# Kernel tuning notes

Hardware: AMD Instinct MI355X
Metric: run time of the kernel (lower is better)

The kernel has to match this reference:

```python
import jax, jax.numpy as jnp
import numpy as np

CODEBOOK_SIZE = 4096
CODE_DIM = 256
N = 65536
COMMITMENT_COST = 0.25


def setup_inputs() -> dict:
    key = jax.random.key(0)
    k1, k2 = jax.random.split(key)
    z_flat = jax.random.normal(k1, (N, CODE_DIM), dtype=jnp.float32)
    # embedding initialized uniform(-1/codebook_size, 1/codebook_size) as in torch module
    emb_weight = jax.random.uniform(
        k2, (CODEBOOK_SIZE, CODE_DIM), dtype=jnp.float32,
        minval=-1.0 / CODEBOOK_SIZE, maxval=1.0 / CODEBOOK_SIZE)
    return {"z_flat": z_flat, "emb_weight": emb_weight}


def reference(z_flat, emb_weight):
    # squared L2 distances: [N, K] = |z|^2 + |e|^2 - 2 z e^T
    distances = (
        jnp.sum(z_flat ** 2, axis=1, keepdims=True)
        + jnp.sum(emb_weight ** 2, axis=1)
        - 2.0 * jnp.matmul(z_flat, emb_weight.T)
    )
    indices = jnp.argmin(distances, axis=1)  # [N]
    quantized = emb_weight[indices]          # [N, code_dim]

    e_latent_loss = jnp.mean((jax.lax.stop_gradient(quantized) - z_flat) ** 2)
    q_latent_loss = jnp.mean((quantized - jax.lax.stop_gradient(z_flat)) ** 2)
    loss = q_latent_loss + COMMITMENT_COST * e_latent_loss

    # straight-through estimator
    quantized_st = z_flat + jax.lax.stop_gradient(quantized - z_flat)
    return (loss, quantized_st, indices)
```

## Files before the change

### kernel.cpp

```cpp
#include <hip/hip_runtime.h>

#define KCODES 4096
#define DIM    256
#define NROWS  65536
#define MARGIN 4.0e-4f
#define DSLACK 3.0e-5f
#define LCAP   4096
#define CPAD   32
#define LSTRIDE (DIM + 4)

typedef unsigned long long u64;
typedef unsigned int  uint;
typedef unsigned short ushort;
typedef __attribute__((ext_vector_type(8))) short bf16x8;
typedef __attribute__((ext_vector_type(4))) float f32x4;

typedef __attribute__((address_space(3))) uint lds_u32_t;
typedef __attribute__((address_space(1))) uint glb_u32_t;

__device__ __forceinline__ void g2lds16(const void* g, void* l) {
    __builtin_amdgcn_global_load_lds((const glb_u32_t*)g, (lds_u32_t*)l, 16, 0, 0);
}

__device__ __forceinline__ float dppmin_quad(float m) {
    m = fminf(m, __int_as_float(__builtin_amdgcn_update_dpp(0, __float_as_int(m), 0xB1, 0xF, 0xF, true)));
    m = fminf(m, __int_as_float(__builtin_amdgcn_update_dpp(0, __float_as_int(m), 0x4E, 0xF, 0xF, true)));
    return m;
}
__device__ __forceinline__ float dppmin_row16(float m) {
    m = fminf(m, __int_as_float(__builtin_amdgcn_update_dpp(0, __float_as_int(m), 0x124, 0xF, 0xF, true)));
    m = fminf(m, __int_as_float(__builtin_amdgcn_update_dpp(0, __float_as_int(m), 0x128, 0xF, 0xF, true)));
    return m;
}
__device__ __forceinline__ uint dppor_row16(uint v) {
    v |= (uint)__builtin_amdgcn_update_dpp(0, (int)v, 0x124, 0xF, 0xF, true);
    v |= (uint)__builtin_amdgcn_update_dpp(0, (int)v, 0x128, 0xF, 0xF, true);
    return v;
}


__device__ __forceinline__ float np_half_sum128(const float4* __restrict__ p4) {
    #pragma clang fp contract(off)
    float4 v0 = p4[0], v1 = p4[1];
    float r0 = v0.x * v0.x, r1 = v0.y * v0.y, r2 = v0.z * v0.z, r3 = v0.w * v0.w;
    float r4 = v1.x * v1.x, r5 = v1.y * v1.y, r6 = v1.z * v1.z, r7 = v1.w * v1.w;
    #pragma unroll
    for (int i = 1; i < 16; ++i) {
        float4 a = p4[2 * i], b = p4[2 * i + 1];
        r0 += a.x * a.x; r1 += a.y * a.y; r2 += a.z * a.z; r3 += a.w * a.w;
        r4 += b.x * b.x; r5 += b.y * b.y; r6 += b.z * b.z; r7 += b.w * b.w;
    }
    return ((r0 + r1) + (r2 + r3)) + ((r4 + r5) + (r6 + r7));
}

__global__ void k_rownorm(const float* __restrict__ src, float* __restrict__ dst, int nrows) {
    int r = blockIdx.x * blockDim.x + threadIdx.x;
    if (r >= nrows) return;
    const float4* p4 = (const float4*)(src + (size_t)r * DIM);
    float s;
    {
        #pragma clang fp contract(off)
        s = np_half_sum128(p4) + np_half_sum128(p4 + 32);
    }
    dst[r] = s;
}

__device__ __forceinline__ float f32_dist(float Cr, float ebc, double accv) {
    #pragma clang fp contract(off)
    float A = Cr + ebc;
    float B = 2.0f * (float)accv;
    return A - B;
}

__device__ __forceinline__ ushort f2bf(float f) {
    uint u = __float_as_uint(f);
    return (ushort)((u + 0x7fffu + ((u >> 16) & 1u)) >> 16);
}

__device__ __forceinline__ uint4 pack8(float4 a, float4 b) {
    uint4 ov;
    ov.x = (uint)f2bf(a.x) | ((uint)f2bf(a.y) << 16);
    ov.y = (uint)f2bf(a.z) | ((uint)f2bf(a.w) << 16);
    ov.z = (uint)f2bf(b.x) | ((uint)f2bf(b.y) << 16);
    ov.w = (uint)f2bf(b.z) | ((uint)f2bf(b.w) << 16);
    return ov;
}


__global__ void k_prep(const float* __restrict__ src, ushort* __restrict__ dst,
                       float* __restrict__ nrm, int nrows) {
    int r = blockIdx.x * blockDim.x + threadIdx.x;
    if (r >= nrows) return;
    const float4* p4 = (const float4*)(src + (size_t)r * DIM);
    uint4* d4 = (uint4*)(dst + (size_t)r * DIM);
    float h[2];
    #pragma unroll
    for (int half = 0; half < 2; ++half) {
        #pragma clang fp contract(off)
        const float4* p = p4 + half * 32;
        float4 v0 = p[0], v1 = p[1];
        d4[half * 16] = pack8(v0, v1);
        float r0 = v0.x * v0.x, r1 = v0.y * v0.y, r2 = v0.z * v0.z, r3 = v0.w * v0.w;
        float r4 = v1.x * v1.x, r5 = v1.y * v1.y, r6 = v1.z * v1.z, r7 = v1.w * v1.w;
        #pragma unroll
        for (int i = 1; i < 16; ++i) {
            float4 a = p[2 * i], b = p[2 * i + 1];
            d4[half * 16 + i] = pack8(a, b);
            r0 += a.x * a.x; r1 += a.y * a.y; r2 += a.z * a.z; r3 += a.w * a.w;
            r4 += b.x * b.x; r5 += b.y * b.y; r6 += b.z * b.z; r7 += b.w * b.w;
        }
        h[half] = ((r0 + r1) + (r2 + r3)) + ((r4 + r5) + (r6 + r7));
    }
    {
        #pragma clang fp contract(off)
        nrm[r] = h[0] + h[1];
    }
}

__global__ void k_init(int* __restrict__ cnt) {
    cnt[blockIdx.x * 256 + threadIdx.x] = 0;
}

__global__ __launch_bounds__(256, 2)
void k_gemm(const ushort* __restrict__ zh, const ushort* __restrict__ eh,
            const float* __restrict__ Crow, const float* __restrict__ eb2,
            float* __restrict__ tk, uint* __restrict__ tk2,
            int* __restrict__ cnt, int* __restrict__ list,
            u64* __restrict__ fkey) {
    __shared__ __align__(16) ushort Bs[2][64 * 256];

    const int t = threadIdx.x;
    const int lane = t & 63;
    const int w = t >> 6;
    const int l15 = lane & 15, l4 = lane >> 4;
    const int row0w = blockIdx.x * 128 + w * 32;

    const char* ebp = (const char*)eh;

    auto stage = [&](int buf, int ct2) {
        const char* base = ebp + (size_t)ct2 * 64 * 512;
        #pragma unroll
        for (int i = 0; i < 8; ++i) {
            int idx = i * 256 + t;
            int code = idx >> 5;
            int c16  = idx & 31;
            int src  = (code << 9) + ((c16 ^ (code & 7)) << 4);
            g2lds16(base + src, (char*)Bs[buf] + idx * 16);
        }
    };

    bf16x8 a[2][8];
    #pragma unroll
    for (int f = 0; f < 2; ++f)
        #pragma unroll
        for (int ks = 0; ks < 8; ++ks)
            a[f][ks] = *(const bf16x8*)&zh[(size_t)(row0w + f * 16 + l15) * 256 + ks * 32 + l4 * 8];

    float crf[8];
    #pragma unroll
    for (int f = 0; f < 2; ++f)
        #pragma unroll
        for (int rg = 0; rg < 4; ++rg)
            crf[f * 4 + rg] = Crow[row0w + f * 16 + l4 * 4 + rg];

    float mprev[8];
    const f32x4 fzero = (f32x4){0.f, 0.f, 0.f, 0.f};
    f32x4 accA[2][4], accB[2][4];
    float ebvA[4], ebvB[4];

    auto ksloop = [&](const ushort* Bb, f32x4 (&acc)[2][4]) {
        #pragma unroll
        for (int ks = 0; ks < 8; ++ks) {
            bf16x8 bfv[4];
            #pragma unroll
            for (int cg = 0; cg < 4; ++cg) {
                int rB = cg * 16 + l15;
                int off = rB * 256 + ((ks * 32 + l4 * 8) ^ ((l15 & 7) << 3));
                bfv[cg] = *(const bf16x8*)&Bb[off];
            }
            __builtin_amdgcn_s_setprio(1);
            #pragma unroll
            for (int f = 0; f < 2; ++f)
                #pragma unroll
                for (int cg = 0; cg < 4; ++cg)
                    acc[f][cg] = __builtin_amdgcn_mfma_f32_16x16x32_bf16(
                        a[f][ks], bfv[cg], ks == 0 ? fzero : acc[f][cg], 0, 0, 0);
            __builtin_amdgcn_s_setprio(0);
        }
    };

    auto epi = [&](f32x4 (&acc)[2][4], const float (&ebv)[4], int ct2, bool odd) {
        #pragma unroll
        for (int f = 0; f < 2; ++f) {
            #pragma unroll
            for (int rg = 0; rg < 4; ++rg) {
                float m =    fmaf(-2.0f, acc[f][0][rg], ebv[0]);
                m = fminf(m, fmaf(-2.0f, acc[f][1][rg], ebv[1]));
                m = fminf(m, fmaf(-2.0f, acc[f][2][rg], ebv[2]));
                m = fminf(m, fmaf(-2.0f, acc[f][3][rg], ebv[3]));
                m = dppmin_quad(m);
                if (!odd) {
                    mprev[f * 4 + rg] = m;
                } else {
                    m = fminf(m, mprev[f * 4 + rg]);
                    float mt = dppmin_row16(m);
                    int q = (int)((m - mt) * 1e5f);
                    q = q > 255 ? 255 : q;
                    uint pk = (uint)q << (8 * (l15 >> 2));
                    pk = dppor_row16(pk);
                    if (l15 == 0) {
                        int grow = row0w + f * 16 + l4 * 4 + rg;
                        int tt = ct2 >> 1;
                        tk [(size_t)tt * NROWS + grow] = crf[f * 4 + rg] + mt;
                        tk2[(size_t)tt * NROWS + grow] = pk;
                    }
                }
            }
        }
    };

    stage(0, 0);
    #pragma unroll
    for (int cg = 0; cg < 4; ++cg) ebvA[cg] = eb2[cg * 16 + l15];
    __syncthreads();

    for (int tp = 0; tp < 32; ++tp) {
        int t0 = 2 * tp;
        stage(1, t0 + 1);
        if (tp > 0) epi(accB, ebvB, t0 - 1, true);
        ksloop(Bs[0], accA);
        __syncthreads();

        if (tp < 31) stage(0, t0 + 2);
        #pragma unroll
        for (int cg = 0; cg < 4; ++cg) ebvB[cg] = eb2[(t0 + 1) * 64 + cg * 16 + l15];
        epi(accA, ebvA, t0, false);
        if (tp < 31) {
            #pragma unroll
            for (int cg = 0; cg < 4; ++cg) ebvA[cg] = eb2[(t0 + 2) * 64 + cg * 16 + l15];
        }
        ksloop(Bs[1], accB);
        __syncthreads();
    }
    epi(accB, ebvB, 63, true);

    __syncthreads();
    if (t < 128) {
        int row = blockIdx.x * 128 + t;
        float tm[32]; uint pkv[32];
        #pragma unroll
        for (int tt = 0; tt < 32; ++tt) {
            tm[tt]  = tk [(size_t)tt * NROWS + row];
            pkv[tt] = tk2[(size_t)tt * NROWS + row];
        }
        float best = tm[0];
        #pragma unroll
        for (int tt = 1; tt < 32; ++tt) best = fminf(best, tm[tt]);
        fkey[row] = ~0ull;
        float cutoff = best + (MARGIN + DSLACK);
        #pragma unroll
        for (int tt = 0; tt < 32; ++tt) {
            #pragma unroll
            for (int p = 0; p < 4; ++p) {
                float v = tm[tt] + (float)((pkv[tt] >> (8 * p)) & 255u) * 1e-5f;
                bool pred = v <= cutoff;
                u64 mask = __ballot(pred);
                if (mask) {
                    int sub = tt * 4 + p;
                    int nq = __popcll(mask);
                    int rank = __popcll(mask & ((1ull << lane) - 1ull));
                    int base = 0;
                    if (lane == 0) base = atomicAdd(&cnt[sub * CPAD], nq);
                    base = __shfl(base, 0, 64);
                    int pos = base + rank;
                    if (pred && pos < LCAP) list[sub * LCAP + pos] = row;
                }
            }
        }
    }
}

__global__ __launch_bounds__(256, 2)
void k_exact(const float* __restrict__ z, const float* __restrict__ e,
             const float* __restrict__ Crow, const float* __restrict__ eb2,
             const int* __restrict__ list, const int* __restrict__ cnt,
             u64* __restrict__ fkey) {
    __shared__ __align__(16) float ex[32][260];
    __shared__ __align__(16) float zx[32][260];
    __shared__ int rows[32];
    __shared__ u64 keytab[32][17];
    const int sub = blockIdx.x;
    const int tile = sub >> 2, qq = sub & 3;
    const int nct = cnt[sub * CPAD];
    const int t = threadIdx.x;
    const int rp = t & 15, cs = t >> 4;

    {
        int cc = t >> 3, c8 = t & 7;
        int gcode = tile * 128 + (cc >> 2) * 16 + qq * 4 + (cc & 3);
        const float4* src = (const float4*)(e + (size_t)gcode * DIM);
        float4* dr = (float4*)ex[cc];
        #pragma unroll
        for (int j = 0; j < 8; ++j) dr[c8 + 8 * j] = src[c8 + 8 * j];
    }
    const int gc0 = tile * 128 + (cs >> 2) * 16 + qq * 4 + (cs & 3);
    const int gc1 = tile * 128 + ((cs >> 2) + 4) * 16 + qq * 4 + (cs & 3);
    const float ebc0 = eb2[gc0];
    const float ebc1 = eb2[gc1];

    for (int base = blockIdx.y * 32; base < nct; base += gridDim.y * 32) {
        __syncthreads();
        if (t < 32) {
            int i = base + t;
            rows[t] = list[sub * LCAP + (i < nct ? i : nct - 1)];
        }
        __syncthreads();
        {
            int rr = t >> 3, c8 = t & 7;
            const float4* src = (const float4*)(z + (size_t)rows[rr] * DIM);
            float4* dr = (float4*)zx[rr];
            #pragma unroll
            for (int j = 0; j < 8; ++j) dr[c8 + 8 * j] = src[c8 + 8 * j];
        }
        __syncthreads();

        double a00 = 0.0, a01 = 0.0, a10 = 0.0, a11 = 0.0;
        const float4* z0 = (const float4*)zx[rp];
        const float4* z1 = (const float4*)zx[rp + 16];
        const float4* e0 = (const float4*)ex[cs];
        const float4* e1 = (const float4*)ex[cs + 16];
        #pragma unroll 8
        for (int d4 = 0; d4 < 64; ++d4) {
            float4 x0 = z0[d4], x1 = z1[d4], y0 = e0[d4], y1 = e1[d4];
            a00 += (double)x0.x * (double)y0.x; a00 += (double)x0.y * (double)y0.y;
            a00 += (double)x0.z * (double)y0.z; a00 += (double)x0.w * (double)y0.w;
            a01 += (double)x0.x * (double)y1.x; a01 += (double)x0.y * (double)y1.y;
            a01 += (double)x0.z * (double)y1.z; a01 += (double)x0.w * (double)y1.w;
            a10 += (double)x1.x * (double)y0.x; a10 += (double)x1.y * (double)y0.y;
            a10 += (double)x1.z * (double)y0.z; a10 += (double)x1.w * (double)y0.w;
            a11 += (double)x1.x * (double)y1.x; a11 += (double)x1.y * (double)y1.y;
            a11 += (double)x1.z * (double)y1.z; a11 += (double)x1.w * (double)y1.w;
        }
        int r0 = rows[rp], r1 = rows[rp + 16];
        float C0 = Crow[r0], C1 = Crow[r1];
        u64 k00 = ((u64)__float_as_uint(f32_dist(C0, ebc0, a00)) << 32) | (u64)gc0;
        u64 k01 = ((u64)__float_as_uint(f32_dist(C0, ebc1, a01)) << 32) | (u64)gc1;
        u64 k10 = ((u64)__float_as_uint(f32_dist(C1, ebc0, a10)) << 32) | (u64)gc0;
        u64 k11 = ((u64)__float_as_uint(f32_dist(C1, ebc1, a11)) << 32) | (u64)gc1;
        keytab[rp][cs]      = k00 < k01 ? k00 : k01;
        keytab[rp + 16][cs] = k10 < k11 ? k10 : k11;
        __syncthreads();
        if (t < 32) {
            u64 kb = keytab[t][0];
            #pragma unroll
            for (int j = 1; j < 16; ++j) {
                u64 k = keytab[t][j];
                kb = k < kb ? k : kb;
            }
            atomicMin((unsigned long long*)&fkey[rows[t]], kb);
        }
    }
}

__global__ __launch_bounds__(256)
void k_gather(const float* __restrict__ z, const float* __restrict__ e,
              const u64* __restrict__ fkey, float* __restrict__ out,
              double* __restrict__ partial) {
    __shared__ double lred[4];
    const int t = threadIdx.x;
    const int row = blockIdx.x * 32 + (t >> 3);
    const int c8 = t & 7;
    const int idx = (int)(fkey[row] & 0xffffffffull);
    if (c8 == 0) out[1 + (size_t)NROWS * DIM + row] = (float)idx;
    const float4* zr = (const float4*)(z + (size_t)row * DIM);
    const float4* er = (const float4*)(e + (size_t)idx * DIM);
    float4* orow = (float4*)(out + 1 + (size_t)row * DIM);
    double lacc = 0.0;
    #pragma unroll
    for (int j = 0; j < 8; ++j) {
        float4 q = er[c8 + 8 * j];
        float4 zv = zr[c8 + 8 * j];
        orow[c8 + 8 * j] = q;
        double d0 = (double)q.x - (double)zv.x;
        double d1 = (double)q.y - (double)zv.y;
        double d2 = (double)q.z - (double)zv.z;
        double d3 = (double)q.w - (double)zv.w;
        lacc += d0 * d0 + d1 * d1 + d2 * d2 + d3 * d3;
    }
    for (int off = 32; off > 0; off >>= 1) lacc += __shfl_down(lacc, off, 64);
    if ((t & 63) == 0) lred[t >> 6] = lacc;
    __syncthreads();
    if (t == 0) partial[blockIdx.x] = lred[0] + lred[1] + lred[2] + lred[3];
}

__global__ void k_finish(const double* __restrict__ partial, float* __restrict__ out, int n) {
    __shared__ double s[256];
    double a = 0.0;
    for (int i = threadIdx.x; i < n; i += 256) a += partial[i];
    s[threadIdx.x] = a;
    __syncthreads();
    for (int off = 128; off > 0; off >>= 1) {
        if (threadIdx.x < off) s[threadIdx.x] += s[threadIdx.x + off];
        __syncthreads();
    }
    if (threadIdx.x == 0)
        out[0] = (float)(1.25 * s[0] / ((double)NROWS * (double)DIM));
}


__global__ __launch_bounds__(256, 1)
void k_main_slow(const float* __restrict__ z, const float* __restrict__ e,
                 const float* __restrict__ Crow, const float* __restrict__ eb2,
                 float* __restrict__ out, double* __restrict__ partial) {
    __shared__ float  zt[64][LSTRIDE];
    __shared__ float  et[64][LSTRIDE];
    __shared__ float  redd[64][17];
    __shared__ int    redi[64][17];
    __shared__ int    bsel[64];
    __shared__ double lred[4];

    const int t  = threadIdx.x;
    const int tx = t & 15;
    const int ty = t >> 4;
    const int row0 = blockIdx.x * 64;

    {
        const float4* zsrc = (const float4*)(z + (size_t)row0 * DIM);
        for (int i = t; i < 64 * (DIM / 4); i += 256) {
            int r = i >> 6, c4 = i & 63;
            *(float4*)&zt[r][c4 * 4] = zsrc[r * (DIM / 4) + c4];
        }
    }
    float Cr[4];
    #pragma unroll
    for (int ri = 0; ri < 4; ++ri) Cr[ri] = Crow[row0 + ty * 4 + ri];
    float bestd[4]; int besti[4];
    #pragma unroll
    for (int ri = 0; ri < 4; ++ri) { bestd[ri] = __int_as_float(0x7f800000); besti[ri] = 0; }

    for (int kt = 0; kt < KCODES / 64; ++kt) {
        __syncthreads();
        {
            const float4* esrc = (const float4*)(e + (size_t)kt * 64 * DIM);
            for (int i = t; i < 64 * (DIM / 4); i += 256) {
                int r = i >> 6, c4 = i & 63;
                *(float4*)&et[r][c4 * 4] = esrc[r * (DIM / 4) + c4];
            }
        }
        __syncthreads();
        double acc[4][4];
        #pragma unroll
        for (int a = 0; a < 4; ++a)
            #pragma unroll
            for (int b = 0; b < 4; ++b) acc[a][b] = 0.0;
        #pragma unroll 4
        for (int d4 = 0; d4 < DIM / 4; ++d4) {
            float4 za[4], ea[4];
            #pragma unroll
            for (int ri = 0; ri < 4; ++ri) za[ri] = *(const float4*)&zt[ty * 4 + ri][d4 * 4];
            #pragma unroll
            for (int ci = 0; ci < 4; ++ci) ea[ci] = *(const float4*)&et[tx + 16 * ci][d4 * 4];
            #pragma unroll
            for (int ri = 0; ri < 4; ++ri)
                #pragma unroll
                for (int ci = 0; ci < 4; ++ci)
                    acc[ri][ci] += (double)za[ri].x * (double)ea[ci].x
                                 + (double)za[ri].y * (double)ea[ci].y
                                 + (double)za[ri].z * (double)ea[ci].z
                                 + (double)za[ri].w * (double)ea[ci].w;
        }
        #pragma unroll
        for (int ci = 0; ci < 4; ++ci) {
            int c = kt * 64 + tx + 16 * ci;
            float ebc = eb2[c];
            #pragma unroll
            for (int ri = 0; ri < 4; ++ri) {
                float d = f32_dist(Cr[ri], ebc, acc[ri][ci]);
                if (d < bestd[ri]) { bestd[ri] = d; besti[ri] = c; }
            }
        }
    }
    __syncthreads();
    #pragma unroll
    for (int ri = 0; ri < 4; ++ri) {
        redd[ty * 4 + ri][tx] = bestd[ri];
        redi[ty * 4 + ri][tx] = besti[ri];
    }
    __syncthreads();
    if (t < 64) {
        float bd = redd[t][0]; int bi = redi[t][0];
        for (int j = 1; j < 16; ++j) {
            float d = redd[t][j]; int i2 = redi[t][j];
            if (d < bd || (d == bd && i2 < bi)) { bd = d; bi = i2; }
        }
        bsel[t] = bi;
        out[1 + (size_t)NROWS * DIM + row0 + t] = (float)bi;
    }
    __syncthreads();
    double lacc = 0.0;
    {
        int r = t >> 2, qd = (t & 3) * 64;
        int bi = bsel[r];
        const float* qrow = e + (size_t)bi * DIM + qd;
        float* orow = out + 1 + (size_t)(row0 + r) * DIM + qd;
        #pragma unroll 4
        for (int d = 0; d < 64; ++d) {
            float qv = qrow[d], zv = zt[r][qd + d];
            double df = (double)qv - (double)zv;
            lacc += df * df;
            orow[d] = qv;
        }
    }
    for (int off = 32; off > 0; off >>= 1) lacc += __shfl_down(lacc, off, 64);
    if ((t & 63) == 0) lred[t >> 6] = lacc;
    __syncthreads();
    if (t == 0) partial[blockIdx.x] = lred[0] + lred[1] + lred[2] + lred[3];
}


extern "C" void kernel_launch(void* const* d_in, const int* in_sizes, int n_in,
                              void* d_out, int out_size, void* d_ws, size_t ws_size,
                              hipStream_t stream) {
    const float* z = (const float*)d_in[0];
    const float* e = (const float*)d_in[1];
    float* out = (float*)d_out;
    char* w = (char*)d_ws;

    size_t o = 0;
    auto take = [&](size_t b) { size_t r = o; o = (o + b + 255) & ~(size_t)255; return r; };
    size_t o_zh = take((size_t)NROWS * DIM * 2);
    size_t o_eh = take((size_t)KCODES * DIM * 2);
    size_t o_cr = take((size_t)NROWS * 4);
    size_t o_eb = take((size_t)KCODES * 4);
    size_t o_tk = take((size_t)32 * NROWS * 4);
    size_t o_t2 = take((size_t)32 * NROWS * 4);
    size_t o_fk = take((size_t)NROWS * 8);
    size_t o_cn = take((size_t)128 * CPAD * 4);
    size_t o_ls = take((size_t)128 * LCAP * 4);
    size_t o_pt = take((size_t)2048 * 8);
    size_t need = o;

    if (ws_size >= need) {
        ushort* zh = (ushort*)(w + o_zh);
        ushort* eh = (ushort*)(w + o_eh);
        float* Cr  = (float*)(w + o_cr);
        float* eb  = (float*)(w + o_eb);
        float* tk  = (float*)(w + o_tk);
        uint*  tk2 = (uint*)(w + o_t2);
        u64*   fk  = (u64*)(w + o_fk);
        int*   cn  = (int*)(w + o_cn);
        int*   ls  = (int*)(w + o_ls);
        double* pt = (double*)(w + o_pt);

        k_prep<<<NROWS / 256, 256, 0, stream>>>(z, zh, Cr, NROWS);
        k_prep<<<KCODES / 256, 256, 0, stream>>>(e, eh, eb, KCODES);
        k_init<<<(128 * CPAD) / 256, 256, 0, stream>>>(cn);
        k_gemm<<<NROWS / 128, 256, 0, stream>>>(zh, eh, Cr, eb, tk, tk2, cn, ls, fk);
        dim3 ge(128, 16);
        k_exact<<<ge, 256, 0, stream>>>(z, e, Cr, eb, ls, cn, fk);
        k_gather<<<NROWS / 32, 256, 0, stream>>>(z, e, fk, out, pt);
        k_finish<<<1, 256, 0, stream>>>(pt, out, 2048);
    } else {
        float* Cr  = (float*)w;
        float* eb  = Cr + NROWS;
        double* pt = (double*)(eb + KCODES);
        k_rownorm<<<NROWS / 256, 256, 0, stream>>>(z, Cr, NROWS);
        k_rownorm<<<KCODES / 256, 256, 0, stream>>>(e, eb, KCODES);
        k_main_slow<<<NROWS / 64, 256, 0, stream>>>(z, e, Cr, eb, out, pt);
        k_finish<<<1, 256, 0, stream>>>(pt, out, NROWS / 64);
    }
}
```

Before: 331.4 us.

## Double rows per GEMM wave, prefetch B fragments, split candidate-list build into kernel

New measurement: 370.1 us. 11.7% more time.

```diff
diff --git a/kernel.cpp b/kernel.cpp
--- a/kernel.cpp
+++ b/kernel.cpp
@@ -121,19 +121,17 @@
     cnt[blockIdx.x * 256 + threadIdx.x] = 0;
 }
 
-__global__ __launch_bounds__(256, 2)
+__global__ __launch_bounds__(256, 1)
 void k_gemm(const ushort* __restrict__ zh, const ushort* __restrict__ eh,
             const float* __restrict__ Crow, const float* __restrict__ eb2,
-            float* __restrict__ tk, uint* __restrict__ tk2,
-            int* __restrict__ cnt, int* __restrict__ list,
-            u64* __restrict__ fkey) {
+            float* __restrict__ tk, uint* __restrict__ tk2) {
     __shared__ __align__(16) ushort Bs[2][64 * 256];
 
     const int t = threadIdx.x;
     const int lane = t & 63;
     const int w = t >> 6;
     const int l15 = lane & 15, l4 = lane >> 4;
-    const int row0w = blockIdx.x * 128 + w * 32;
+    const int row0w = blockIdx.x * 256 + w * 64;
 
     const char* ebp = (const char*)eh;
 
@@ -149,49 +147,57 @@
         }
     };
 
-    bf16x8 a[2][8];
-    #pragma unroll
-    for (int f = 0; f < 2; ++f)
+    bf16x8 a[4][8];
+    #pragma unroll
+    for (int f = 0; f < 4; ++f)
         #pragma unroll
         for (int ks = 0; ks < 8; ++ks)
             a[f][ks] = *(const bf16x8*)&zh[(size_t)(row0w + f * 16 + l15) * 256 + ks * 32 + l4 * 8];
 
-    float crf[8];
-    #pragma unroll
-    for (int f = 0; f < 2; ++f)
+    float crf[16];
+    #pragma unroll
+    for (int f = 0; f < 4; ++f)
         #pragma unroll
         for (int rg = 0; rg < 4; ++rg)
             crf[f * 4 + rg] = Crow[row0w + f * 16 + l4 * 4 + rg];
 
-    float mprev[8];
+    float mprev[16];
     const f32x4 fzero = (f32x4){0.f, 0.f, 0.f, 0.f};
-    f32x4 accA[2][4], accB[2][4];
+    f32x4 accA[4][4], accB[4][4];
     float ebvA[4], ebvB[4];
 
-    auto ksloop = [&](const ushort* Bb, f32x4 (&acc)[2][4]) {
+    auto readB = [&](const ushort* Bb, int ks, int cg) -> bf16x8 {
+        int rB = cg * 16 + l15;
+        int off = rB * 256 + ((ks * 32 + l4 * 8) ^ ((l15 & 7) << 3));
+        return *(const bf16x8*)&Bb[off];
+    };
+
+    auto ksloop = [&](const ushort* Bb, f32x4 (&acc)[4][4]) {
+        bf16x8 bva[4], bvb[4];
+        #pragma unroll
+        for (int cg = 0; cg < 4; ++cg) bva[cg] = readB(Bb, 0, cg);
         #pragma unroll
         for (int ks = 0; ks < 8; ++ks) {
-            bf16x8 bfv[4];
-            #pragma unroll
-            for (int cg = 0; cg < 4; ++cg) {
-                int rB = cg * 16 + l15;
-                int off = rB * 256 + ((ks * 32 + l4 * 8) ^ ((l15 & 7) << 3));
-                bfv[cg] = *(const bf16x8*)&Bb[off];
+            const bf16x8* cur = (ks & 1) ? bvb : bva;
+            bf16x8*       nxt = (ks & 1) ? bva : bvb;
+            if (ks < 7) {
+                #pragma unroll
+                for (int cg = 0; cg < 4; ++cg) nxt[cg] = readB(Bb, ks + 1, cg);
             }
             __builtin_amdgcn_s_setprio(1);
             #pragma unroll
-            for (int f = 0; f < 2; ++f)
+            for (int f = 0; f < 4; ++f)
                 #pragma unroll
                 for (int cg = 0; cg < 4; ++cg)
                     acc[f][cg] = __builtin_amdgcn_mfma_f32_16x16x32_bf16(
-                        a[f][ks], bfv[cg], ks == 0 ? fzero : acc[f][cg], 0, 0, 0);
+                        a[f][ks], cur[cg], ks == 0 ? fzero : acc[f][cg], 0, 0, 0);
             __builtin_amdgcn_s_setprio(0);
         }
     };
 
-    auto epi = [&](f32x4 (&acc)[2][4], const float (&ebv)[4], int ct2, bool odd) {
-        #pragma unroll
-        for (int f = 0; f < 2; ++f) {
+    auto epi = [&](f32x4 (&acc)[4][4], const float (&ebv)[4], int ct2, bool odd) {
+        #pragma unroll
+        for (int f = 0; f < 4; ++f) {
             #pragma unroll
             for (int rg = 0; rg < 4; ++rg) {
                 float m =    fmaf(-2.0f, acc[f][0][rg], ebv[0]);
@@ -243,38 +249,41 @@
         __syncthreads();
     }
     epi(accB, ebvB, 63, true);
-
-    __syncthreads();
-    if (t < 128) {
-        int row = blockIdx.x * 128 + t;
-        float tm[32]; uint pkv[32];
-        #pragma unroll
-        for (int tt = 0; tt < 32; ++tt) {
-            tm[tt]  = tk [(size_t)tt * NROWS + row];
-            pkv[tt] = tk2[(size_t)tt * NROWS + row];
-        }
-        float best = tm[0];
-        #pragma unroll
-        for (int tt = 1; tt < 32; ++tt) best = fminf(best, tm[tt]);
-        fkey[row] = ~0ull;
-        float cutoff = best + (MARGIN + DSLACK);
-        #pragma unroll
-        for (int tt = 0; tt < 32; ++tt) {
-            #pragma unroll
-            for (int p = 0; p < 4; ++p) {
-                float v = tm[tt] + (float)((pkv[tt] >> (8 * p)) & 255u) * 1e-5f;
-                bool pred = v <= cutoff;
-                u64 mask = __ballot(pred);
-                if (mask) {
-                    int sub = tt * 4 + p;
-                    int nq = __popcll(mask);
-                    int rank = __popcll(mask & ((1ull << lane) - 1ull));
-                    int base = 0;
-                    if (lane == 0) base = atomicAdd(&cnt[sub * CPAD], nq);
-                    base = __shfl(base, 0, 64);
-                    int pos = base + rank;
-                    if (pred && pos < LCAP) list[sub * LCAP + pos] = row;
-                }
+}
+
+__global__ void k_lists(const float* __restrict__ tk, const uint* __restrict__ tk2,
+                        int* __restrict__ cnt, int* __restrict__ list,
+                        u64* __restrict__ fkey) {
+    int row = blockIdx.x * 256 + threadIdx.x;
+    int lane = threadIdx.x & 63;
+    float tm[32]; uint pk[32];
+    #pragma unroll
+    for (int tt = 0; tt < 32; ++tt) {
+        tm[tt] = tk [(size_t)tt * NROWS + row];
+        pk[tt] = tk2[(size_t)tt * NROWS + row];
+    }
+    float best = tm[0];
+    #pragma unroll
+    for (int tt = 1; tt < 32; ++tt) best = fminf(best, tm[tt]);
+    fkey[row] = ~0ull;
+    float cutoff = best + (MARGIN + DSLACK);
+
+    #pragma unroll
+    for (int tt = 0; tt < 32; ++tt) {
+        #pragma unroll
+        for (int p = 0; p < 4; ++p) {
+            float v = tm[tt] + (float)((pk[tt] >> (8 * p)) & 255u) * 1e-5f;
+            bool pred = v <= cutoff;
+            u64 mask = __ballot(pred);
+            if (mask) {
+                int sub = tt * 4 + p;
+                int nq = __popcll(mask);
+                int rank = __popcll(mask & ((1ull << lane) - 1ull));
+                int base = 0;
+                if (lane == 0) base = atomicAdd(&cnt[sub * CPAD], nq);
+                base = __shfl(base, 0, 64);
+                int pos = base + rank;
+                if (pred && pos < LCAP) list[sub * LCAP + pos] = row;
             }
         }
     }
@@ -555,7 +564,8 @@
         k_prep<<<NROWS / 256, 256, 0, stream>>>(z, zh, Cr, NROWS);
         k_prep<<<KCODES / 256, 256, 0, stream>>>(e, eh, eb, KCODES);
         k_init<<<(128 * CPAD) / 256, 256, 0, stream>>>(cn);
-        k_gemm<<<NROWS / 128, 256, 0, stream>>>(zh, eh, Cr, eb, tk, tk2, cn, ls, fk);
+        k_gemm<<<NROWS / 256, 256, 0, stream>>>(zh, eh, Cr, eb, tk, tk2);
+        k_lists<<<NROWS / 256, 256, 0, stream>>>(tk, tk2, cn, ls, fk);
         dim3 ge(128, 16);
         k_exact<<<ge, 256, 0, stream>>>(z, e, Cr, eb, ls, cn, fk);
         k_gather<<<NROWS / 32, 256, 0, stream>>>(z, e, fk, out, pt);
```

## Refine candidate filtering to 2-code groups and split list building into separate kernel

Applied to the files above, without the earlier changes.

Measured after the change: 334.5 us. About the same (+0.9%).

```diff
diff --git a/kernel.cpp b/kernel.cpp
--- a/kernel.cpp
+++ b/kernel.cpp
@@ -4,7 +4,8 @@
 #define DIM    256
 #define NROWS  65536
 #define MARGIN 4.0e-4f
-#define DSLACK 3.0e-5f
+#define DSLACK 4.0e-5f
+#define QDELT  4.0e-5f
 #define LCAP   4096
 #define CPAD   32
 #define LSTRIDE (DIM + 4)
@@ -22,17 +23,20 @@
     __builtin_amdgcn_global_load_lds((const glb_u32_t*)g, (lds_u32_t*)l, 16, 0, 0);
 }
 
-__device__ __forceinline__ float dppmin_quad(float m) {
+__device__ __forceinline__ float dppmin_pair(float m) {
+    m = fminf(m, __int_as_float(__builtin_amdgcn_update_dpp(0, __float_as_int(m), 0xB1, 0xF, 0xF, true)));
+    return m;
+}
+__device__ __forceinline__ float dppmin_row16(float m) {
     m = fminf(m, __int_as_float(__builtin_amdgcn_update_dpp(0, __float_as_int(m), 0xB1, 0xF, 0xF, true)));
     m = fminf(m, __int_as_float(__builtin_amdgcn_update_dpp(0, __float_as_int(m), 0x4E, 0xF, 0xF, true)));
-    return m;
-}
-__device__ __forceinline__ float dppmin_row16(float m) {
     m = fminf(m, __int_as_float(__builtin_amdgcn_update_dpp(0, __float_as_int(m), 0x124, 0xF, 0xF, true)));
     m = fminf(m, __int_as_float(__builtin_amdgcn_update_dpp(0, __float_as_int(m), 0x128, 0xF, 0xF, true)));
     return m;
 }
 __device__ __forceinline__ uint dppor_row16(uint v) {
+    v |= (uint)__builtin_amdgcn_update_dpp(0, (int)v, 0xB1, 0xF, 0xF, true);
+    v |= (uint)__builtin_amdgcn_update_dpp(0, (int)v, 0x4E, 0xF, 0xF, true);
     v |= (uint)__builtin_amdgcn_update_dpp(0, (int)v, 0x124, 0xF, 0xF, true);
     v |= (uint)__builtin_amdgcn_update_dpp(0, (int)v, 0x128, 0xF, 0xF, true);
     return v;
@@ -124,9 +128,7 @@
 __global__ __launch_bounds__(256, 2)
 void k_gemm(const ushort* __restrict__ zh, const ushort* __restrict__ eh,
             const float* __restrict__ Crow, const float* __restrict__ eb2,
-            float* __restrict__ tk, uint* __restrict__ tk2,
-            int* __restrict__ cnt, int* __restrict__ list,
-            u64* __restrict__ fkey) {
+            float* __restrict__ tk, uint* __restrict__ tk2) {
     __shared__ __align__(16) ushort Bs[2][64 * 256];
 
     const int t = threadIdx.x;
@@ -198,15 +200,15 @@
                 m = fminf(m, fmaf(-2.0f, acc[f][1][rg], ebv[1]));
                 m = fminf(m, fmaf(-2.0f, acc[f][2][rg], ebv[2]));
                 m = fminf(m, fmaf(-2.0f, acc[f][3][rg], ebv[3]));
-                m = dppmin_quad(m);
+                m = dppmin_pair(m);
                 if (!odd) {
                     mprev[f * 4 + rg] = m;
                 } else {
                     m = fminf(m, mprev[f * 4 + rg]);
                     float mt = dppmin_row16(m);
-                    int q = (int)((m - mt) * 1e5f);
-                    q = q > 255 ? 255 : q;
-                    uint pk = (uint)q << (8 * (l15 >> 2));
+                    int q = (int)((m - mt) * 2.5e4f);
+                    q = q > 15 ? 15 : q;
+                    uint pk = (uint)q << (4 * (l15 >> 1));
                     pk = dppor_row16(pk);
                     if (l15 == 0) {
                         int grow = row0w + f * 16 + l4 * 4 + rg;
@@ -243,38 +245,41 @@
         __syncthreads();
     }
     epi(accB, ebvB, 63, true);
-
-    __syncthreads();
-    if (t < 128) {
-        int row = blockIdx.x * 128 + t;
-        float tm[32]; uint pkv[32];
-        #pragma unroll
-        for (int tt = 0; tt < 32; ++tt) {
-            tm[tt]  = tk [(size_t)tt * NROWS + row];
-            pkv[tt] = tk2[(size_t)tt * NROWS + row];
-        }
-        float best = tm[0];
-        #pragma unroll
-        for (int tt = 1; tt < 32; ++tt) best = fminf(best, tm[tt]);
-        fkey[row] = ~0ull;
-        float cutoff = best + (MARGIN + DSLACK);
-        #pragma unroll
-        for (int tt = 0; tt < 32; ++tt) {
-            #pragma unroll
-            for (int p = 0; p < 4; ++p) {
-                float v = tm[tt] + (float)((pkv[tt] >> (8 * p)) & 255u) * 1e-5f;
-                bool pred = v <= cutoff;
-                u64 mask = __ballot(pred);
-                if (mask) {
-                    int sub = tt * 4 + p;
-                    int nq = __popcll(mask);
-                    int rank = __popcll(mask & ((1ull << lane) - 1ull));
-                    int base = 0;
-                    if (lane == 0) base = atomicAdd(&cnt[sub * CPAD], nq);
-                    base = __shfl(base, 0, 64);
-                    int pos = base + rank;
-                    if (pred && pos < LCAP) list[sub * LCAP + pos] = row;
-                }
+}
+
+__global__ void k_lists(const float* __restrict__ tk, const uint* __restrict__ tk2,
+                        int* __restrict__ cnt, int* __restrict__ list,
+                        u64* __restrict__ fkey) {
+    int row = blockIdx.x * 256 + threadIdx.x;
+    int lane = threadIdx.x & 63;
+    float tm[32]; uint pk[32];
+    #pragma unroll
+    for (int tt = 0; tt < 32; ++tt) {
+        tm[tt] = tk [(size_t)tt * NROWS + row];
+        pk[tt] = tk2[(size_t)tt * NROWS + row];
+    }
+    float best = tm[0];
+    #pragma unroll
+    for (int tt = 1; tt < 32; ++tt) best = fminf(best, tm[tt]);
+    fkey[row] = ~0ull;
+    float cutoff = best + (MARGIN + DSLACK);
+
+    #pragma unroll
+    for (int tt = 0; tt < 32; ++tt) {
+        #pragma unroll
+        for (int p = 0; p < 8; ++p) {
+            float v = tm[tt] + (float)((pk[tt] >> (4 * p)) & 15u) * QDELT;
+            bool pred = v <= cutoff;
+            u64 mask = __ballot(pred);
+            if (mask) {
+                int sub = tt * 8 + p;
+                int nq = __popcll(mask);
+                int rank = __popcll(mask & ((1ull << lane) - 1ull));
+                int base = 0;
+                if (lane == 0) base = atomicAdd(&cnt[sub * CPAD], nq);
+                base = __shfl(base, 0, 64);
+                int pos = base + rank;
+                if (pred && pos < LCAP) list[sub * LCAP + pos] = row;
             }
         }
     }
@@ -285,28 +290,26 @@
              const float* __restrict__ Crow, const float* __restrict__ eb2,
              const int* __restrict__ list, const int* __restrict__ cnt,
              u64* __restrict__ fkey) {
-    __shared__ __align__(16) float ex[32][260];
+    __shared__ __align__(16) float ex[16][260];
     __shared__ __align__(16) float zx[32][260];
     __shared__ int rows[32];
     __shared__ u64 keytab[32][17];
     const int sub = blockIdx.x;
-    const int tile = sub >> 2, qq = sub & 3;
+    const int tile = sub >> 3, p2 = sub & 7;
     const int nct = cnt[sub * CPAD];
     const int t = threadIdx.x;
     const int rp = t & 15, cs = t >> 4;
 
     {
-        int cc = t >> 3, c8 = t & 7;
-        int gcode = tile * 128 + (cc >> 2) * 16 + qq * 4 + (cc & 3);
+        int cc = t >> 4, c8 = t & 15;
+        int gcode = tile * 128 + (cc >> 3) * 64 + ((cc >> 1) & 3) * 16 + p2 * 2 + (cc & 1);
         const float4* src = (const float4*)(e + (size_t)gcode * DIM);
         float4* dr = (float4*)ex[cc];
         #pragma unroll
-        for (int j = 0; j < 8; ++j) dr[c8 + 8 * j] = src[c8 + 8 * j];
-    }
-    const int gc0 = tile * 128 + (cs >> 2) * 16 + qq * 4 + (cs & 3);
-    const int gc1 = tile * 128 + ((cs >> 2) + 4) * 16 + qq * 4 + (cs & 3);
+        for (int j = 0; j < 4; ++j) dr[c8 + 16 * j] = src[c8 + 16 * j];
+    }
+    const int gc0 = tile * 128 + (cs >> 3) * 64 + ((cs >> 1) & 3) * 16 + p2 * 2 + (cs & 1);
     const float ebc0 = eb2[gc0];
-    const float ebc1 = eb2[gc1];
 
     for (int base = blockIdx.y * 32; base < nct; base += gridDim.y * 32) {
         __syncthreads();
@@ -324,31 +327,22 @@
         }
         __syncthreads();
 
-        double a00 = 0.0, a01 = 0.0, a10 = 0.0, a11 = 0.0;
+        double a0 = 0.0, a1 = 0.0;
         const float4* z0 = (const float4*)zx[rp];
         const float4* z1 = (const float4*)zx[rp + 16];
         const float4* e0 = (const float4*)ex[cs];
-        const float4* e1 = (const float4*)ex[cs + 16];
         #pragma unroll 8
         for (int d4 = 0; d4 < 64; ++d4) {
-            float4 x0 = z0[d4], x1 = z1[d4], y0 = e0[d4], y1 = e1[d4];
-            a00 += (double)x0.x * (double)y0.x; a00 += (double)x0.y * (double)y0.y;
-            a00 += (double)x0.z * (double)y0.z; a00 += (double)x0.w * (double)y0.w;
-            a01 += (double)x0.x * (double)y1.x; a01 += (double)x0.y * (double)y1.y;
-            a01 += (double)x0.z * (double)y1.z; a01 += (double)x0.w * (double)y1.w;
-            a10 += (double)x1.x * (double)y0.x; a10 += (double)x1.y * (double)y0.y;
-            a10 += (double)x1.z * (double)y0.z; a10 += (double)x1.w * (double)y0.w;
-            a11 += (double)x1.x * (double)y1.x; a11 += (double)x1.y * (double)y1.y;
-            a11 += (double)x1.z * (double)y1.z; a11 += (double)x1.w * (double)y1.w;
+            float4 x0 = z0[d4], x1 = z1[d4], y0 = e0[d4];
+            a0 += (double)x0.x * (double)y0.x; a0 += (double)x0.y * (double)y0.y;
+            a0 += (double)x0.z * (double)y0.z; a0 += (double)x0.w * (double)y0.w;
+            a1 += (double)x1.x * (double)y0.x; a1 += (double)x1.y * (double)y0.y;
+            a1 += (double)x1.z * (double)y0.z; a1 += (double)x1.w * (double)y0.w;
         }
         int r0 = rows[rp], r1 = rows[rp + 16];
         float C0 = Crow[r0], C1 = Crow[r1];
-        u64 k00 = ((u64)__float_as_uint(f32_dist(C0, ebc0, a00)) << 32) | (u64)gc0;
-        u64 k01 = ((u64)__float_as_uint(f32_dist(C0, ebc1, a01)) << 32) | (u64)gc1;
-        u64 k10 = ((u64)__float_as_uint(f32_dist(C1, ebc0, a10)) << 32) | (u64)gc0;
-        u64 k11 = ((u64)__float_as_uint(f32_dist(C1, ebc1, a11)) << 32) | (u64)gc1;
-        keytab[rp][cs]      = k00 < k01 ? k00 : k01;
-        keytab[rp + 16][cs] = k10 < k11 ? k10 : k11;
+        keytab[rp][cs]      = ((u64)__float_as_uint(f32_dist(C0, ebc0, a0)) << 32) | (u64)gc0;
+        keytab[rp + 16][cs] = ((u64)__float_as_uint(f32_dist(C1, ebc0, a1)) << 32) | (u64)gc0;
         __syncthreads();
         if (t < 32) {
             u64 kb = keytab[t][0];
@@ -535,8 +529,8 @@
     size_t o_tk = take((size_t)32 * NROWS * 4);
     size_t o_t2 = take((size_t)32 * NROWS * 4);
     size_t o_fk = take((size_t)NROWS * 8);
-    size_t o_cn = take((size_t)128 * CPAD * 4);
-    size_t o_ls = take((size_t)128 * LCAP * 4);
+    size_t o_cn = take((size_t)256 * CPAD * 4);
+    size_t o_ls = take((size_t)256 * LCAP * 4);
     size_t o_pt = take((size_t)2048 * 8);
     size_t need = o;
 
@@ -554,9 +548,10 @@
 
         k_prep<<<NROWS / 256, 256, 0, stream>>>(z, zh, Cr, NROWS);
         k_prep<<<KCODES / 256, 256, 0, stream>>>(e, eh, eb, KCODES);
-        k_init<<<(128 * CPAD) / 256, 256, 0, stream>>>(cn);
-        k_gemm<<<NROWS / 128, 256, 0, stream>>>(zh, eh, Cr, eb, tk, tk2, cn, ls, fk);
-        dim3 ge(128, 16);
+        k_init<<<(256 * CPAD) / 256, 256, 0, stream>>>(cn);
+        k_gemm<<<NROWS / 128, 256, 0, stream>>>(zh, eh, Cr, eb, tk, tk2);
+        k_lists<<<NROWS / 256, 256, 0, stream>>>(tk, tk2, cn, ls, fk);
+        dim3 ge(256, 8);
         k_exact<<<ge, 256, 0, stream>>>(z, e, Cr, eb, ls, cn, fk);
         k_gather<<<NROWS / 32, 256, 0, stream>>>(z, e, fk, out, pt);
         k_finish<<<1, 256, 0, stream>>>(pt, out, 2048);
```

## Split candidate-list build into own kernel; derive loss from stored exact distances

Applied to the files above, without the earlier changes.

Result: no change. 328.5 us (-0.9%).

```diff
diff --git a/kernel.cpp b/kernel.cpp
--- a/kernel.cpp
+++ b/kernel.cpp
@@ -124,9 +124,7 @@
 __global__ __launch_bounds__(256, 2)
 void k_gemm(const ushort* __restrict__ zh, const ushort* __restrict__ eh,
             const float* __restrict__ Crow, const float* __restrict__ eb2,
-            float* __restrict__ tk, uint* __restrict__ tk2,
-            int* __restrict__ cnt, int* __restrict__ list,
-            u64* __restrict__ fkey) {
+            float* __restrict__ tk, uint* __restrict__ tk2) {
     __shared__ __align__(16) ushort Bs[2][64 * 256];
 
     const int t = threadIdx.x;
@@ -243,38 +241,41 @@
         __syncthreads();
     }
     epi(accB, ebvB, 63, true);
-
-    __syncthreads();
-    if (t < 128) {
-        int row = blockIdx.x * 128 + t;
-        float tm[32]; uint pkv[32];
-        #pragma unroll
-        for (int tt = 0; tt < 32; ++tt) {
-            tm[tt]  = tk [(size_t)tt * NROWS + row];
-            pkv[tt] = tk2[(size_t)tt * NROWS + row];
-        }
-        float best = tm[0];
-        #pragma unroll
-        for (int tt = 1; tt < 32; ++tt) best = fminf(best, tm[tt]);
-        fkey[row] = ~0ull;
-        float cutoff = best + (MARGIN + DSLACK);
-        #pragma unroll
-        for (int tt = 0; tt < 32; ++tt) {
-            #pragma unroll
-            for (int p = 0; p < 4; ++p) {
-                float v = tm[tt] + (float)((pkv[tt] >> (8 * p)) & 255u) * 1e-5f;
-                bool pred = v <= cutoff;
-                u64 mask = __ballot(pred);
-                if (mask) {
-                    int sub = tt * 4 + p;
-                    int nq = __popcll(mask);
-                    int rank = __popcll(mask & ((1ull << lane) - 1ull));
-                    int base = 0;
-                    if (lane == 0) base = atomicAdd(&cnt[sub * CPAD], nq);
-                    base = __shfl(base, 0, 64);
-                    int pos = base + rank;
-                    if (pred && pos < LCAP) list[sub * LCAP + pos] = row;
-                }
+}
+
+__global__ void k_lists(const float* __restrict__ tk, const uint* __restrict__ tk2,
+                        int* __restrict__ cnt, int* __restrict__ list,
+                        u64* __restrict__ fkey) {
+    int row = blockIdx.x * 256 + threadIdx.x;
+    int lane = threadIdx.x & 63;
+    float tm[32]; uint pk[32];
+    #pragma unroll
+    for (int tt = 0; tt < 32; ++tt) {
+        tm[tt] = tk [(size_t)tt * NROWS + row];
+        pk[tt] = tk2[(size_t)tt * NROWS + row];
+    }
+    float best = tm[0];
+    #pragma unroll
+    for (int tt = 1; tt < 32; ++tt) best = fminf(best, tm[tt]);
+    fkey[row] = ~0ull;
+    float cutoff = best + (MARGIN + DSLACK);
+
+    #pragma unroll
+    for (int tt = 0; tt < 32; ++tt) {
+        #pragma unroll
+        for (int p = 0; p < 4; ++p) {
+            float v = tm[tt] + (float)((pk[tt] >> (8 * p)) & 255u) * 1e-5f;
+            bool pred = v <= cutoff;
+            u64 mask = __ballot(pred);
+            if (mask) {
+                int sub = tt * 4 + p;
+                int nq = __popcll(mask);
+                int rank = __popcll(mask & ((1ull << lane) - 1ull));
+                int base = 0;
+                if (lane == 0) base = atomicAdd(&cnt[sub * CPAD], nq);
+                base = __shfl(base, 0, 64);
+                int pos = base + rank;
+                if (pred && pos < LCAP) list[sub * LCAP + pos] = row;
             }
         }
     }
@@ -363,34 +364,30 @@
 }
 
 __global__ __launch_bounds__(256)
-void k_gather(const float* __restrict__ z, const float* __restrict__ e,
-              const u64* __restrict__ fkey, float* __restrict__ out,
-              double* __restrict__ partial) {
-    __shared__ double lred[4];
+void k_gather(const float* __restrict__ e, const u64* __restrict__ fkey,
+              float* __restrict__ out, double* __restrict__ partial) {
+    __shared__ double s[32];
     const int t = threadIdx.x;
     const int row = blockIdx.x * 32 + (t >> 3);
     const int c8 = t & 7;
-    const int idx = (int)(fkey[row] & 0xffffffffull);
+    u64 key = fkey[row];
+    const int idx = (int)(key & 0xffffffffull);
     if (c8 == 0) out[1 + (size_t)NROWS * DIM + row] = (float)idx;
-    const float4* zr = (const float4*)(z + (size_t)row * DIM);
     const float4* er = (const float4*)(e + (size_t)idx * DIM);
     float4* orow = (float4*)(out + 1 + (size_t)row * DIM);
-    double lacc = 0.0;
-    #pragma unroll
-    for (int j = 0; j < 8; ++j) {
-        float4 q = er[c8 + 8 * j];
-        float4 zv = zr[c8 + 8 * j];
-        orow[c8 + 8 * j] = q;
-        double d0 = (double)q.x - (double)zv.x;
-        double d1 = (double)q.y - (double)zv.y;
-        double d2 = (double)q.z - (double)zv.z;
-        double d3 = (double)q.w - (double)zv.w;
-        lacc += d0 * d0 + d1 * d1 + d2 * d2 + d3 * d3;
-    }
-    for (int off = 32; off > 0; off >>= 1) lacc += __shfl_down(lacc, off, 64);
-    if ((t & 63) == 0) lred[t >> 6] = lacc;
-    __syncthreads();
-    if (t == 0) partial[blockIdx.x] = lred[0] + lred[1] + lred[2] + lred[3];
+    #pragma unroll
+    for (int j = 0; j < 8; ++j) orow[c8 + 8 * j] = er[c8 + 8 * j];
+    if (t < 32) {
+        u64 k2 = fkey[blockIdx.x * 32 + t];
+        s[t] = (double)__uint_as_float((uint)(k2 >> 32));
+    }
+    __syncthreads();
+    if (t == 0) {
+        double a = 0.0;
+        #pragma unroll
+        for (int i = 0; i < 32; ++i) a += s[i];
+        partial[blockIdx.x] = a;
+    }
 }
 
 __global__ void k_finish(const double* __restrict__ partial, float* __restrict__ out, int n) {
@@ -555,10 +552,11 @@
         k_prep<<<NROWS / 256, 256, 0, stream>>>(z, zh, Cr, NROWS);
         k_prep<<<KCODES / 256, 256, 0, stream>>>(e, eh, eb, KCODES);
         k_init<<<(128 * CPAD) / 256, 256, 0, stream>>>(cn);
-        k_gemm<<<NROWS / 128, 256, 0, stream>>>(zh, eh, Cr, eb, tk, tk2, cn, ls, fk);
+        k_gemm<<<NROWS / 128, 256, 0, stream>>>(zh, eh, Cr, eb, tk, tk2);
+        k_lists<<<NROWS / 256, 256, 0, stream>>>(tk, tk2, cn, ls, fk);
         dim3 ge(128, 16);
         k_exact<<<ge, 256, 0, stream>>>(z, e, Cr, eb, ls, cn, fk);
-        k_gather<<<NROWS / 32, 256, 0, stream>>>(z, e, fk, out, pt);
+        k_gather<<<NROWS / 32, 256, 0, stream>>>(e, fk, out, pt);
         k_finish<<<1, 256, 0, stream>>>(pt, out, 2048);
     } else {
         float* Cr  = (float*)w;
```
